# Kernel optimization log

Measured on AMD Instinct MI355X. Metric: run time of the kernel, lower is better.

The kernel has to match this reference:

```python
import jax, jax.numpy as jnp
from jax import lax
import numpy as np

B, CIN, H, W = 8, 3, 256, 256
ED, NH, WS, SHIFT = 64, 4, 8, 4
HD = ED // NH
MLP_H = 4 * ED
N = WS * WS
NW = (H // WS) * (W // WS)
EPS = 1e-5


def _attn_mask():
    # Static shifted-window attention mask, computed with numpy (H, W, WS, SHIFT are static).
    img = np.zeros((H, W), np.float32)
    sl = [slice(0, -WS), slice(-WS, -SHIFT), slice(-SHIFT, None)]
    cnt = 0
    for hs in sl:
        for ws_ in sl:
            img[hs, ws_] = cnt
            cnt += 1
    mw = img.reshape(H // WS, WS, W // WS, WS).transpose(0, 2, 1, 3).reshape(-1, N)
    d = mw[:, None, :] - mw[:, :, None]  # (NW, N, N)
    return jnp.asarray(np.where(d != 0, -100.0, 0.0).astype(np.float32))

ATTN_MASK = _attn_mask()


def _ln(x, g, b):
    m = x.mean(-1, keepdims=True)
    v = x.var(-1, keepdims=True)
    return (x - m) / jnp.sqrt(v + EPS) * g + b


def _conv3x3(x, w, b):
    y = lax.conv_general_dilated(x, w, (1, 1), 'SAME',
                                 dimension_numbers=('NCHW', 'OIHW', 'NCHW'))
    return y + b[None, :, None, None]


def setup_inputs() -> dict:
    key = jax.random.key(0)
    ks = jax.random.split(key, 20)
    s = 0.02
    return dict(
        x=jax.random.normal(ks[0], (B, CIN, H, W), jnp.float32),
        conv_e_w=jax.random.normal(ks[1], (ED, CIN, 3, 3), jnp.float32) * s,
        conv_e_b=jnp.zeros((ED,), jnp.float32),
        n1_g=jnp.ones((ED,), jnp.float32),
        n1_b=jnp.zeros((ED,), jnp.float32),
        qkv_w=jax.random.normal(ks[2], (3 * ED, ED), jnp.float32) * s,
        qkv_b=jnp.zeros((3 * ED,), jnp.float32),
        proj_w=jax.random.normal(ks[3], (ED, ED), jnp.float32) * s,
        proj_b=jnp.zeros((ED,), jnp.float32),
        n2_g=jnp.ones((ED,), jnp.float32),
        n2_b=jnp.zeros((ED,), jnp.float32),
        fc1_w=jax.random.normal(ks[4], (MLP_H, ED), jnp.float32) * s,
        fc1_b=jnp.zeros((MLP_H,), jnp.float32),
        fc2_w=jax.random.normal(ks[5], (ED, MLP_H), jnp.float32) * s,
        fc2_b=jnp.zeros((ED,), jnp.float32),
        conv_u_w=jax.random.normal(ks[6], (CIN, ED, 3, 3), jnp.float32) * s,
        conv_u_b=jnp.zeros((CIN,), jnp.float32),
    )


def reference(x, conv_e_w, conv_e_b, n1_g, n1_b, qkv_w, qkv_b, proj_w, proj_b,
              n2_g, n2_b, fc1_w, fc1_b, fc2_w, fc2_b, conv_u_w, conv_u_b):
    scale = HD ** -0.5
    # conv embed -> NHWC
    xe = _conv3x3(x, conv_e_w, conv_e_b).transpose(0, 2, 3, 1)  # (B,H,W,ED)
    xs = jnp.roll(xe, (-SHIFT, -SHIFT), axis=(1, 2))
    # window partition -> (B*NW, N, ED)
    xw = xs.reshape(B, H // WS, WS, W // WS, WS, ED).transpose(0, 1, 3, 2, 4, 5)
    xw = xw.reshape(B * NW, N, ED)
    # windowed MHA
    xn = _ln(xw, n1_g, n1_b)
    qkv = (xn @ qkv_w.T + qkv_b).reshape(B * NW, N, 3, NH, HD).transpose(2, 0, 3, 1, 4)
    q, k, v = qkv[0] * scale, qkv[1], qkv[2]  # (B*NW, NH, N, HD)
    attn = jnp.einsum('bhnd,bhmd->bhnm', q, k)
    attn = attn.reshape(B, NW, NH, N, N) + ATTN_MASK[None, :, None]
    attn = jax.nn.softmax(attn.reshape(B * NW, NH, N, N), axis=-1)
    out = jnp.einsum('bhnm,bhmd->bhnd', attn, v)
    out = out.transpose(0, 2, 1, 3).reshape(B * NW, N, ED) @ proj_w.T + proj_b
    xw = xw + out
    # window reverse -> (B,H,W,ED), roll back
    xr = xw.reshape(B, H // WS, W // WS, WS, WS, ED).transpose(0, 1, 3, 2, 4, 5)
    xr = xr.reshape(B, H, W, ED)
    x_out = jnp.roll(xr, (SHIFT, SHIFT), axis=(1, 2))  # NHWC
    # MLP branch with residual
    xm = _ln(x_out.reshape(-1, ED), n2_g, n2_b)
    xm = jax.nn.gelu(xm @ fc1_w.T + fc1_b, approximate=False)
    xm = (xm @ fc2_w.T + fc2_b).reshape(B, H, W, ED)
    x_final = (x_out + xm).transpose(0, 3, 1, 2)  # NCHW
    recon = _conv3x3(x_final, conv_u_w, conv_u_b)
    return x + recon
```

## Files before the change

### kernel.cpp

```cpp
#include <hip/hip_runtime.h>
#include <hip/hip_bf16.h>
#include <math.h>

using bf16 = __hip_bfloat16;

typedef short s16x8 __attribute__((ext_vector_type(8)));
typedef short s16x4 __attribute__((ext_vector_type(4)));
typedef float f32x4 __attribute__((ext_vector_type(4)));

static __device__ __forceinline__ float s2f(short s) {
    return __uint_as_float(((unsigned)(unsigned short)s) << 16);
}
static __device__ __forceinline__ short f2s(float v) {
    bf16 b = __float2bfloat16(v);
    return *reinterpret_cast<short*>(&b);
}
static __device__ __forceinline__ float b2f(bf16 v) { return __bfloat162float(v); }
static __device__ __forceinline__ bf16  f2b(float v) { return __float2bfloat16(v); }
static __device__ __forceinline__ unsigned pack2(float a, float b) {
    return (unsigned)(unsigned short)f2s(a) | ((unsigned)(unsigned short)f2s(b) << 16);
}
static __device__ __forceinline__ float frcp(float x) {
    return __builtin_amdgcn_rcpf(x);
}

static __device__ __forceinline__ int lswz(int row, int col) {
    return row * 64 + ((((col >> 3) ^ row) & 7) << 3) + (col & 7);
}
static __device__ __forceinline__ int lbase(int row, int col) {
    return row * 64 + ((((col >> 3) ^ row) & 7) << 3);
}
static __device__ __forceinline__ s16x8 ld8(const short* p) {
    return *(const s16x8*)p;
}
static __device__ __forceinline__ f32x4 mfma16(s16x8 a, s16x8 b, f32x4 c) {
    return __builtin_amdgcn_mfma_f32_16x16x32_bf16(a, b, c, 0, 0, 0);
}

constexpr int B_   = 8;
constexpr int CIN_ = 3;
constexpr int H_   = 256;
constexpr int W_   = 256;
constexpr int ED_  = 64;
constexpr float EPS_ = 1e-5f;

constexpr int WQ_OFF  = 0;
constexpr int WP_OFF  = 12288;
constexpr int W1_OFF  = 16384;
constexpr int W2_OFF  = 32768;
constexpr int NFRAG   = 96;

static __device__ __forceinline__ int clsf(int tok, int eh, int ew) {
    int ch = eh ? (1 + ((tok >> 3) >= 4)) : 0;
    int cw = ew ? (1 + ((tok & 7) >= 4)) : 0;
    return ch * 3 + cw;
}

__global__ __launch_bounds__(256) void k_prep(
    const float* __restrict__ qkvw, const float* __restrict__ projw,
    const float* __restrict__ fc1w, const float* __restrict__ fc2w,
    short* __restrict__ wb)
{
    int g    = blockIdx.x * 256 + threadIdx.x;
    int l    = g & 63;
    int frag = g >> 6;
    int lr   = l & 15, lhi = l >> 4;

    const float* src;
    if (frag < 24) {
        int blk = frag >> 1, half = frag & 1;
        src = qkvw + (blk * 16 + lr) * 64 + half * 32 + lhi * 8;
    } else if (frag < 32) {
        int f = frag - 24; int blk = f >> 1, half = f & 1;
        src = projw + (blk * 16 + lr) * 64 + half * 32 + lhi * 8;
    } else if (frag < 64) {
        int f = frag - 32; int blk = f >> 1, half = f & 1;
        src = fc1w + (blk * 16 + lr) * 64 + half * 32 + lhi * 8;
    } else {
        int f = frag - 64; int pair = f >> 1, half = f & 1;
        int k = pair >> 2, nt = pair & 3;
        src = fc2w + (nt * 16 + lr) * 256 + k * 64 + half * 32 + lhi * 8;
    }
    float4 v0 = *(const float4*)src;
    float4 v1 = *(const float4*)(src + 4);
    s16x8 o = { f2s(v0.x), f2s(v0.y), f2s(v0.z), f2s(v0.w),
                f2s(v1.x), f2s(v1.y), f2s(v1.z), f2s(v1.w) };
    *(s16x8*)&wb[frag * 512 + l * 8] = o;
}

__global__ __launch_bounds__(256) void k_conv_embed(
    const float* __restrict__ x, const float* __restrict__ we,
    const float* __restrict__ be, bf16* __restrict__ xe)
{
    const int t    = threadIdx.x;
    const int wv   = t >> 6;
    const int lane = t & 63;
    const int hb   = blockIdx.x;
    const int h    = hb & 255;
    const int b    = hb >> 8;
    const int col  = wv * 64 + lane;

    const float* xb = x + (size_t)b * (CIN_ * H_ * W_);

    float xr[27];
#pragma unroll
    for (int ci = 0; ci < 3; ++ci)
#pragma unroll
        for (int kh = 0; kh < 3; ++kh) {
            int hy = h + kh - 1;
#pragma unroll
            for (int kw = 0; kw < 3; ++kw) {
                int wx = col + kw - 1;
                bool ok = ((unsigned)hy < 256u) & ((unsigned)wx < 256u);
                xr[ci * 9 + kh * 3 + kw] = ok ? xb[ci * 65536 + hy * 256 + wx] : 0.f;
            }
        }

    unsigned pk[32];
#pragma unroll 4
    for (int op = 0; op < 32; ++op) {
        float a0 = be[2 * op];
        float a1 = be[2 * op + 1];
        const float* w0 = we + (2 * op) * 27;
#pragma unroll
        for (int k = 0; k < 27; ++k) {
            a0 += xr[k] * w0[k];
            a1 += xr[k] * w0[27 + k];
        }
        pk[op] = pack2(a0, a1);
    }

    size_t pixel = (size_t)hb * 256 + col;
    uint4* dst = (uint4*)((short*)xe + pixel * 64);
#pragma unroll
    for (int i = 0; i < 8; ++i) dst[i] = *(uint4*)&pk[i * 4];
}

__global__ __launch_bounds__(256, 3) void k_attn(
    const bf16* __restrict__ xe, const short* __restrict__ wq,
    const float* __restrict__ qkv_b, const short* __restrict__ wp,
    const float* __restrict__ proj_b, const float* __restrict__ n1_g,
    const float* __restrict__ n1_b, bf16* __restrict__ x_out)
{
    __shared__ short s_x[64 * 64];
    __shared__ short s_q[64 * 64];
    __shared__ short s_k[64 * 64];
    __shared__ short s_vt[64 * 64];

    const int t    = threadIdx.x;
    const int w    = t >> 6;
    const int lane = t & 63;
    const int lr   = lane & 15;
    const int lhi  = lane >> 4;

    const int bi  = blockIdx.x;
    const int b   = bi >> 10;
    const int wh  = (bi >> 5) & 31;
    const int wwi = bi & 31;
    const int eh  = (wh == 31), ew = (wwi == 31);

    const bf16* xeb = xe + (size_t)b * (H_ * W_ * ED_);
    const f32x4 cz = { 0.f, 0.f, 0.f, 0.f };

    {
        int n = t >> 2, q = t & 3;
        int hp = (wh * 8 + (n >> 3) + 4) & 255;
        int wp_ = (wwi * 8 + (n & 7) + 4) & 255;
        const short* src = (const short*)xeb + (hp * 256 + wp_) * 64 + q * 16;
        s16x8 u0 = *(const s16x8*)src;
        s16x8 u1 = *(const s16x8*)(src + 8);
        float v[16];
        float s = 0.f, sq = 0.f;
#pragma unroll
        for (int j = 0; j < 8; ++j) { v[j] = s2f(u0[j]); v[8 + j] = s2f(u1[j]); }
#pragma unroll
        for (int j = 0; j < 16; ++j) { s += v[j]; sq += v[j] * v[j]; }
        s  += __shfl_xor(s, 1);  s  += __shfl_xor(s, 2);
        sq += __shfl_xor(sq, 1); sq += __shfl_xor(sq, 2);
        float m = s * (1.f / 64.f);
        float rstd = rsqrtf(sq * (1.f / 64.f) - m * m + EPS_);
        s16x8 w0, w1;
#pragma unroll
        for (int j = 0; j < 8; ++j) {
            w0[j] = f2s((v[j] - m) * rstd * n1_g[q * 16 + j] + n1_b[q * 16 + j]);
            w1[j] = f2s((v[8 + j] - m) * rstd * n1_g[q * 16 + 8 + j] + n1_b[q * 16 + 8 + j]);
        }
        *(s16x8*)&s_x[lbase(n, q * 16)]     = w0;
        *(s16x8*)&s_x[lbase(n, q * 16 + 8)] = w1;
    }
    __syncthreads();

    {
        int arow = w * 16 + lr;
        s16x8 a0 = ld8(&s_x[lbase(arow, lhi * 8)]);
        s16x8 a1 = ld8(&s_x[lbase(arow, 32 + lhi * 8)]);
#pragma unroll
        for (int nt = 0; nt < 8; ++nt) {
            s16x8 b0 = *(const s16x8*)&wq[(nt * 2 + 0) * 512 + lane * 8];
            s16x8 b1 = *(const s16x8*)&wq[(nt * 2 + 1) * 512 + lane * 8];
            f32x4 c = mfma16(a1, b1, mfma16(a0, b0, cz));
            float bias = qkv_b[nt * 16 + lr];
#pragma unroll
            for (int r = 0; r < 4; ++r) {
                int tok = w * 16 + lhi * 4 + r;
                float val = c[r] + bias;
                if (nt < 4) { val *= 0.25f; s_q[lswz(tok, nt * 16 + lr)] = f2s(val); }
                else        {               s_k[lswz(tok, (nt - 4) * 16 + lr)] = f2s(val); }
            }
        }
        s16x8 av0 = *(const s16x8*)&wq[((8 + w) * 2 + 0) * 512 + lane * 8];
        s16x8 av1 = *(const s16x8*)&wq[((8 + w) * 2 + 1) * 512 + lane * 8];
#pragma unroll
        for (int nt = 0; nt < 4; ++nt) {
            s16x8 b0 = ld8(&s_x[lbase(nt * 16 + lr, lhi * 8)]);
            s16x8 b1 = ld8(&s_x[lbase(nt * 16 + lr, 32 + lhi * 8)]);
            f32x4 c = mfma16(av1, b1, mfma16(av0, b0, cz));
#pragma unroll
            for (int r = 0; r < 4; ++r) {
                int d = w * 16 + lhi * 4 + r;
                s_vt[lswz(d, nt * 16 + lr)] = f2s(c[r] + qkv_b[128 + d]);
            }
        }
    }
    __syncthreads();

    const int h = w;
    uint2 pk[4][4];
    {
        const s16x8 z8 = { 0, 0, 0, 0, 0, 0, 0, 0 };
        s16x8 kb[4];
#pragma unroll
        for (int mt = 0; mt < 4; ++mt)
            kb[mt] = (lhi >= 2) ? z8
                   : ld8(&s_k[lbase(mt * 16 + lr, h * 16 + (lhi & 1) * 8)]);
#pragma unroll
        for (int nt = 0; nt < 4; ++nt) {
            s16x8 qb = ld8(&s_q[lbase(nt * 16 + lr, h * 16 + (lhi & 1) * 8)]);
            f32x4 S[4];
#pragma unroll
            for (int mt = 0; mt < 4; ++mt)
                S[mt] = mfma16(kb[mt], qb, cz);

            if (eh | ew) {
                int qc = clsf(nt * 16 + lr, eh, ew);
#pragma unroll
                for (int mt = 0; mt < 4; ++mt)
#pragma unroll
                    for (int r = 0; r < 4; ++r) {
                        int kc = clsf(mt * 16 + lhi * 4 + r, eh, ew);
                        S[mt][r] += (kc != qc) ? -100.f : 0.f;
                    }
            }
            float mx = -1e30f;
#pragma unroll
            for (int mt = 0; mt < 4; ++mt)
#pragma unroll
                for (int r = 0; r < 4; ++r) mx = fmaxf(mx, S[mt][r]);
            mx = fmaxf(mx, __shfl_xor(mx, 16));
            mx = fmaxf(mx, __shfl_xor(mx, 32));
            float ev[4][4];
            float sm = 0.f;
#pragma unroll
            for (int mt = 0; mt < 4; ++mt)
#pragma unroll
                for (int r = 0; r < 4; ++r) {
                    ev[mt][r] = __expf(S[mt][r] - mx);
                    sm += ev[mt][r];
                }
            sm += __shfl_xor(sm, 16);
            sm += __shfl_xor(sm, 32);
            float inv = frcp(sm);
#pragma unroll
            for (int mt = 0; mt < 4; ++mt) {
                pk[nt][mt].x = pack2(ev[mt][0] * inv, ev[mt][1] * inv);
                pk[nt][mt].y = pack2(ev[mt][2] * inv, ev[mt][3] * inv);
            }
        }
    }

    {
        f32x4 O[4] = { cz, cz, cz, cz };
        const int  srcl2 = lr + 32 * (lhi & 1);
        const bool selhi = (lhi >= 2);
#pragma unroll
        for (int ks = 0; ks < 2; ++ks) {
            s16x8 bv = ld8(&s_vt[lbase(h * 16 + lr, ks * 32 + lhi * 8)]);
#pragma unroll
            for (int mo = 0; mo < 4; ++mo) {
                unsigned lAx = (unsigned)__shfl((int)pk[mo][ks * 2 + 0].x, srcl2);
                unsigned lAy = (unsigned)__shfl((int)pk[mo][ks * 2 + 0].y, srcl2);
                unsigned lBx = (unsigned)__shfl((int)pk[mo][ks * 2 + 1].x, srcl2);
                unsigned lBy = (unsigned)__shfl((int)pk[mo][ks * 2 + 1].y, srcl2);
                unsigned hAx = (unsigned)__shfl((int)pk[mo][ks * 2 + 0].x, srcl2 + 16);
                unsigned hAy = (unsigned)__shfl((int)pk[mo][ks * 2 + 0].y, srcl2 + 16);
                unsigned hBx = (unsigned)__shfl((int)pk[mo][ks * 2 + 1].x, srcl2 + 16);
                unsigned hBy = (unsigned)__shfl((int)pk[mo][ks * 2 + 1].y, srcl2 + 16);
                uint4 pa;
                pa.x = selhi ? lBx : lAx;
                pa.y = selhi ? lBy : lAy;
                pa.z = selhi ? hBx : hAx;
                pa.w = selhi ? hBy : hAy;
                O[mo] = mfma16(*(s16x8*)&pa, bv, O[mo]);
            }
        }
#pragma unroll
        for (int mo = 0; mo < 4; ++mo)
#pragma unroll
            for (int r = 0; r < 4; ++r)
                s_x[lswz(mo * 16 + lhi * 4 + r, h * 16 + lr)] = f2s(O[mo][r]);
    }
    __syncthreads();

    {
        int arow = w * 16 + lr;
        s16x8 a0 = ld8(&s_x[lbase(arow, lhi * 8)]);
        s16x8 a1 = ld8(&s_x[lbase(arow, 32 + lhi * 8)]);
        size_t rowbase[4];
#pragma unroll
        for (int r = 0; r < 4; ++r) {
            int tok = w * 16 + lhi * 4 + r;
            int hp = (wh * 8 + (tok >> 3) + 4) & 255;
            int wpx = (wwi * 8 + (tok & 7) + 4) & 255;
            rowbase[r] = (size_t)(hp * 256 + wpx) * 64;
        }
        const size_t bbase = (size_t)b * (H_ * W_ * ED_);
#pragma unroll
        for (int nt = 0; nt < 4; ++nt) {
            s16x8 b0 = *(const s16x8*)&wp[(nt * 2 + 0) * 512 + lane * 8];
            s16x8 b1 = *(const s16x8*)&wp[(nt * 2 + 1) * 512 + lane * 8];
            f32x4 c = mfma16(a1, b1, mfma16(a0, b0, cz));
            float bias = proj_b[nt * 16 + lr];
#pragma unroll
            for (int r = 0; r < 4; ++r) {
                size_t gi = rowbase[r] + nt * 16 + lr;
                float val = c[r] + bias + b2f(xeb[gi]);
                x_out[bbase + gi] = f2b(val);
            }
        }
    }
}

__global__ __launch_bounds__(512, 4) void k_mlp(
    const bf16* __restrict__ xo, const short* __restrict__ w1,
    const float* __restrict__ fc1_b, const short* __restrict__ w2,
    const float* __restrict__ fc2_b, const float* __restrict__ n2_g,
    const float* __restrict__ n2_b, bf16* __restrict__ xf)
{
    __shared__ short s_x[128 * 64];
    __shared__ short s_h[128 * 64];

    const int t    = threadIdx.x;
    const int w    = t >> 6;
    const int lane = t & 63;
    const int lr   = lane & 15;
    const int lhi  = lane >> 4;
    const size_t tok0 = (size_t)blockIdx.x * 128;
    const short* xos = (const short*)xo;

    {
        int n = t >> 2, q = t & 3;
        const short* src = xos + (tok0 + n) * 64 + q * 16;
        s16x8 u0 = *(const s16x8*)src;
        s16x8 u1 = *(const s16x8*)(src + 8);
        float v[16];
        float s = 0.f, sq = 0.f;
#pragma unroll
        for (int j = 0; j < 8; ++j) { v[j] = s2f(u0[j]); v[8 + j] = s2f(u1[j]); }
#pragma unroll
        for (int j = 0; j < 16; ++j) { s += v[j]; sq += v[j] * v[j]; }
        s  += __shfl_xor(s, 1);  s  += __shfl_xor(s, 2);
        sq += __shfl_xor(sq, 1); sq += __shfl_xor(sq, 2);
        float m = s * (1.f / 64.f);
        float rstd = rsqrtf(sq * (1.f / 64.f) - m * m + EPS_);
        s16x8 w0, w1_;
#pragma unroll
        for (int j = 0; j < 8; ++j) {
            w0[j]  = f2s((v[j] - m) * rstd * n2_g[q * 16 + j] + n2_b[q * 16 + j]);
            w1_[j] = f2s((v[8 + j] - m) * rstd * n2_g[q * 16 + 8 + j] + n2_b[q * 16 + 8 + j]);
        }
        *(s16x8*)&s_x[lbase(n, q * 16)]     = w0;
        *(s16x8*)&s_x[lbase(n, q * 16 + 8)] = w1_;
    }

    const f32x4 cz = { 0.f, 0.f, 0.f, 0.f };
    f32x4 acc[4] = { cz, cz, cz, cz };
    const int arow = w * 16 + lr;

    s16x8 a0 = ld8(&s_x[lbase(arow, lhi * 8)]);
    s16x8 a1 = ld8(&s_x[lbase(arow, 32 + lhi * 8)]);

    for (int k = 0; k < 4; ++k) {
#pragma unroll
        for (int nt = 0; nt < 4; ++nt) {
            const short* bp = &w1[((k * 4 + nt) * 2) * 512 + lane * 8];
            s16x8 b0 = *(const s16x8*)bp;
            s16x8 b1 = *(const s16x8*)(bp + 512);
            f32x4 c = mfma16(a1, b1, mfma16(a0, b0, cz));
            float bias = fc1_b[k * 64 + nt * 16 + lr];
#pragma unroll
            for (int r = 0; r < 4; ++r) {
                float hv = c[r] + bias;
                float u = hv + 0.044715f * hv * hv * hv;
                hv = hv * frcp(1.f + __expf(-1.5957691216f * u));
                s_h[lswz(w * 16 + lhi * 4 + r, nt * 16 + lr)] = f2s(hv);
            }
        }
        s16x8 h0 = ld8(&s_h[lbase(arow, lhi * 8)]);
        s16x8 h1 = ld8(&s_h[lbase(arow, 32 + lhi * 8)]);
#pragma unroll
        for (int nt = 0; nt < 4; ++nt) {
            const short* bp2 = &w2[((k * 4 + nt) * 2) * 512 + lane * 8];
            s16x8 b0 = *(const s16x8*)bp2;
            s16x8 b1 = *(const s16x8*)(bp2 + 512);
            acc[nt] = mfma16(h1, b1, mfma16(h0, b0, acc[nt]));
        }
    }

#pragma unroll
    for (int nt = 0; nt < 4; ++nt) {
        float bias = fc2_b[nt * 16 + lr];
#pragma unroll
        for (int r = 0; r < 4; ++r) {
            int tok = w * 16 + lhi * 4 + r;
            size_t gi = (tok0 + tok) * 64 + nt * 16 + lr;
            float v = acc[nt][r] + bias + s2f(xos[gi]);
            ((short*)xf)[gi] = f2s(v);
        }
    }
}

__global__ __launch_bounds__(256) void k_conv_up(
    const float* __restrict__ x, const bf16* __restrict__ xf,
    const float* __restrict__ wu, const float* __restrict__ bu,
    float* __restrict__ out)
{
    __shared__ short s_t[198 * 64];
    __shared__ short s_bf[1152 * 8];
    __shared__ float s_wu[1728];

    const int t    = threadIdx.x;
    const int pix0 = blockIdx.x * 64;
    const int b    = pix0 >> 16;
    const int h    = (pix0 >> 8) & 255;
    const int w0   = pix0 & 255;

    const short* xfs = (const short*)xf;

    for (int e = t; e < 1584; e += 256) {
        int rc = e >> 3, j8 = e & 7;
        int hy_l = (unsigned)rc / 66u;
        int wx_l = rc - hy_l * 66;
        int hy = h + hy_l - 1;
        int wx = w0 + wx_l - 1;
        s16x8 v = { 0, 0, 0, 0, 0, 0, 0, 0 };
        if (((unsigned)hy < 256u) & ((unsigned)wx < 256u))
            v = *(const s16x8*)&xfs[((size_t)((b * 256 + hy) * 256 + wx)) * 64 + j8 * 8];
        *(s16x8*)&s_t[lbase(rc, j8 * 8)] = v;
    }
    for (int e = t; e < 1728; e += 256) s_wu[e] = wu[e];
    __syncthreads();

    for (int fid = t; fid < 1152; fid += 256) {
        int tap  = fid >> 7;
        int half = (fid >> 6) & 1;
        int ln   = fid & 63;
        int co   = ln & 15;
        s16x8 v = { 0, 0, 0, 0, 0, 0, 0, 0 };
        if (co < 3) {
            int ci0 = half * 32 + (ln >> 4) * 8;
#pragma unroll
            for (int j = 0; j < 8; ++j)
                v[j] = f2s(s_wu[(co * 64 + ci0 + j) * 9 + tap]);
        }
        *(s16x8*)&s_bf[fid * 8] = v;
    }
    __syncthreads();

    const int wv   = t >> 6;
    const int lane = t & 63;
    const int lr   = lane & 15;
    const int lhi  = lane >> 4;

    f32x4 acc = { 0.f, 0.f, 0.f, 0.f };
#pragma unroll
    for (int kh = 0; kh < 3; ++kh)
#pragma unroll
        for (int kw = 0; kw < 3; ++kw) {
            const int tap = kh * 3 + kw;
            const int R   = kh * 66 + wv * 16 + lr + kw;
#pragma unroll
            for (int half = 0; half < 2; ++half) {
                s16x8 a   = ld8(&s_t[lbase(R, half * 32 + lhi * 8)]);
                s16x8 bfr = ld8(&s_bf[((tap * 2 + half) * 64 + lane) * 8]);
                acc = mfma16(a, bfr, acc);
            }
        }

    if (lr < 3) {
        const int co = lr;
        const int wp = wv * 16 + lhi * 4;
        size_t o0 = (size_t)b * 3 * 65536 + (size_t)co * 65536 + (size_t)h * 256 + w0 + wp;
        float4 xv = *(const float4*)&x[o0];
        float bias = bu[co];
        float4 ov;
        ov.x = acc[0] + bias + xv.x;
        ov.y = acc[1] + bias + xv.y;
        ov.z = acc[2] + bias + xv.z;
        ov.w = acc[3] + bias + xv.w;
        *(float4*)&out[o0] = ov;
    }
}

extern "C" void kernel_launch(void* const* d_in, const int* in_sizes, int n_in,
                              void* d_out, int out_size, void* d_ws, size_t ws_size,
                              hipStream_t stream)
{
    const float* x     = (const float*)d_in[0];
    const float* cew   = (const float*)d_in[1];
    const float* ceb   = (const float*)d_in[2];
    const float* n1g   = (const float*)d_in[3];
    const float* n1b   = (const float*)d_in[4];
    const float* qkvw  = (const float*)d_in[5];
    const float* qkvb  = (const float*)d_in[6];
    const float* projw = (const float*)d_in[7];
    const float* projb = (const float*)d_in[8];
    const float* n2g   = (const float*)d_in[9];
    const float* n2b   = (const float*)d_in[10];
    const float* fc1w  = (const float*)d_in[11];
    const float* fc1b  = (const float*)d_in[12];
    const float* fc2w  = (const float*)d_in[13];
    const float* fc2b  = (const float*)d_in[14];
    const float* cuw   = (const float*)d_in[15];
    const float* cub   = (const float*)d_in[16];
    float* out = (float*)d_out;

    const size_t planeElems = (size_t)B_ * H_ * W_ * ED_;
    bf16* xe = (bf16*)d_ws;
    bf16* xo = (bf16*)((char*)d_ws + planeElems * sizeof(bf16));

    short* wb = (short*)d_out;

    hipLaunchKernelGGL(k_prep, dim3(NFRAG * 64 / 256), dim3(256), 0, stream,
                       qkvw, projw, fc1w, fc2w, wb);
    hipLaunchKernelGGL(k_conv_embed, dim3(2048), dim3(256), 0, stream, x, cew, ceb, xe);
    hipLaunchKernelGGL(k_attn,       dim3(8192), dim3(256), 0, stream,
                       xe, wb + WQ_OFF, qkvb, wb + WP_OFF, projb, n1g, n1b, xo);
    hipLaunchKernelGGL(k_mlp,        dim3(4096), dim3(512), 0, stream,
                       xo, wb + W1_OFF, fc1b, wb + W2_OFF, fc2b, n2g, n2b, xe);
    hipLaunchKernelGGL(k_conv_up,    dim3(8192), dim3(256), 0, stream, x, xe, cuw, cub, out);
}
```

Measured before the change: 411.5 us.

## Fuse windowed attention and MLP into one kernel per window

Merges the attention kernel and the MLP kernel so that each 64-token window block runs LN2, fc1+GELU, fc2 and the residual right after the projection. The attention output stays in LDS and registers instead of being written to and re-read from a global bf16 buffer. This removes a full-plane round trip to global memory and one kernel launch. Since the MLP is per token, it is applied before un-rolling, and results are written straight to the rolled positions. In exchange the MLP now runs at the attention kernel's 256-thread, 64-token block granularity instead of 128-token blocks, and register pressure goes up because residual values are held in registers.

```diff
diff --git a/kernel.cpp b/kernel.cpp
--- a/kernel.cpp
+++ b/kernel.cpp
@@ -136,11 +136,14 @@
     for (int i = 0; i < 8; ++i) dst[i] = *(uint4*)&pk[i * 4];
 }
 
-__global__ __launch_bounds__(256, 3) void k_attn(
+__global__ __launch_bounds__(256, 3) void k_attn_mlp(
     const bf16* __restrict__ xe, const short* __restrict__ wq,
     const float* __restrict__ qkv_b, const short* __restrict__ wp,
     const float* __restrict__ proj_b, const float* __restrict__ n1_g,
-    const float* __restrict__ n1_b, bf16* __restrict__ x_out)
+    const float* __restrict__ n1_b, const short* __restrict__ w1,
+    const float* __restrict__ fc1_b, const short* __restrict__ w2,
+    const float* __restrict__ fc2_b, const float* __restrict__ n2_g,
+    const float* __restrict__ n2_b, bf16* __restrict__ xf)
 {
     __shared__ short s_x[64 * 64];
     __shared__ short s_q[64 * 64];
@@ -179,14 +182,14 @@
         sq += __shfl_xor(sq, 1); sq += __shfl_xor(sq, 2);
         float m = s * (1.f / 64.f);
         float rstd = rsqrtf(sq * (1.f / 64.f) - m * m + EPS_);
-        s16x8 w0, w1;
+        s16x8 w0, w1_;
 #pragma unroll
         for (int j = 0; j < 8; ++j) {
-            w0[j] = f2s((v[j] - m) * rstd * n1_g[q * 16 + j] + n1_b[q * 16 + j]);
-            w1[j] = f2s((v[8 + j] - m) * rstd * n1_g[q * 16 + 8 + j] + n1_b[q * 16 + 8 + j]);
+            w0[j]  = f2s((v[j] - m) * rstd * n1_g[q * 16 + j] + n1_b[q * 16 + j]);
+            w1_[j] = f2s((v[8 + j] - m) * rstd * n1_g[q * 16 + 8 + j] + n1_b[q * 16 + 8 + j]);
         }
         *(s16x8*)&s_x[lbase(n, q * 16)]     = w0;
-        *(s16x8*)&s_x[lbase(n, q * 16 + 8)] = w1;
+        *(s16x8*)&s_x[lbase(n, q * 16 + 8)] = w1_;
     }
     __syncthreads();
 
@@ -311,11 +314,12 @@
     }
     __syncthreads();
 
+    size_t rowbase[4];
+    float  valr[4][4];
     {
         int arow = w * 16 + lr;
         s16x8 a0 = ld8(&s_x[lbase(arow, lhi * 8)]);
         s16x8 a1 = ld8(&s_x[lbase(arow, 32 + lhi * 8)]);
-        size_t rowbase[4];
 #pragma unroll
         for (int r = 0; r < 4; ++r) {
             int tok = w * 16 + lhi * 4 + r;
@@ -323,7 +327,6 @@
             int wpx = (wwi * 8 + (tok & 7) + 4) & 255;
             rowbase[r] = (size_t)(hp * 256 + wpx) * 64;
         }
-        const size_t bbase = (size_t)b * (H_ * W_ * ED_);
 #pragma unroll
         for (int nt = 0; nt < 4; ++nt) {
             s16x8 b0 = *(const s16x8*)&wp[(nt * 2 + 0) * 512 + lane * 8];
@@ -332,36 +335,18 @@
             float bias = proj_b[nt * 16 + lr];
 #pragma unroll
             for (int r = 0; r < 4; ++r) {
-                size_t gi = rowbase[r] + nt * 16 + lr;
-                float val = c[r] + bias + b2f(xeb[gi]);
-                x_out[bbase + gi] = f2b(val);
-            }
-        }
-    }
-}
-
-__global__ __launch_bounds__(512, 4) void k_mlp(
-    const bf16* __restrict__ xo, const short* __restrict__ w1,
-    const float* __restrict__ fc1_b, const short* __restrict__ w2,
-    const float* __restrict__ fc2_b, const float* __restrict__ n2_g,
-    const float* __restrict__ n2_b, bf16* __restrict__ xf)
-{
-    __shared__ short s_x[128 * 64];
-    __shared__ short s_h[128 * 64];
-
-    const int t    = threadIdx.x;
-    const int w    = t >> 6;
-    const int lane = t & 63;
-    const int lr   = lane & 15;
-    const int lhi  = lane >> 4;
-    const size_t tok0 = (size_t)blockIdx.x * 128;
-    const short* xos = (const short*)xo;
-
-    {
-        int n = t >> 2, q = t & 3;
-        const short* src = xos + (tok0 + n) * 64 + q * 16;
-        s16x8 u0 = *(const s16x8*)src;
-        s16x8 u1 = *(const s16x8*)(src + 8);
+                int tok = w * 16 + lhi * 4 + r;
+                short vs = f2s(c[r] + bias + b2f(xeb[rowbase[r] + nt * 16 + lr]));
+                s_x[lswz(tok, nt * 16 + lr)] = vs;
+                valr[nt][r] = s2f(vs);
+            }
+        }
+    }
+
+    {
+        int n = w * 16 + (lane >> 2), q = lane & 3;
+        s16x8 u0 = ld8(&s_x[lbase(n, q * 16)]);
+        s16x8 u1 = ld8(&s_x[lbase(n, q * 16 + 8)]);
         float v[16];
         float s = 0.f, sq = 0.f;
 #pragma unroll
@@ -378,53 +363,55 @@
             w0[j]  = f2s((v[j] - m) * rstd * n2_g[q * 16 + j] + n2_b[q * 16 + j]);
             w1_[j] = f2s((v[8 + j] - m) * rstd * n2_g[q * 16 + 8 + j] + n2_b[q * 16 + 8 + j]);
         }
-        *(s16x8*)&s_x[lbase(n, q * 16)]     = w0;
-        *(s16x8*)&s_x[lbase(n, q * 16 + 8)] = w1_;
-    }
-
-    const f32x4 cz = { 0.f, 0.f, 0.f, 0.f };
+        *(s16x8*)&s_q[lbase(n, q * 16)]     = w0;
+        *(s16x8*)&s_q[lbase(n, q * 16 + 8)] = w1_;
+    }
+
     f32x4 acc[4] = { cz, cz, cz, cz };
-    const int arow = w * 16 + lr;
-
-    s16x8 a0 = ld8(&s_x[lbase(arow, lhi * 8)]);
-    s16x8 a1 = ld8(&s_x[lbase(arow, 32 + lhi * 8)]);
-
-    for (int k = 0; k < 4; ++k) {
+    {
+        const int arow = w * 16 + lr;
+        s16x8 xa0 = ld8(&s_q[lbase(arow, lhi * 8)]);
+        s16x8 xa1 = ld8(&s_q[lbase(arow, 32 + lhi * 8)]);
+
+        for (int k = 0; k < 4; ++k) {
+#pragma unroll
+            for (int nt = 0; nt < 4; ++nt) {
+                const short* bp = &w1[((k * 4 + nt) * 2) * 512 + lane * 8];
+                s16x8 b0 = *(const s16x8*)bp;
+                s16x8 b1 = *(const s16x8*)(bp + 512);
+                f32x4 c = mfma16(xa1, b1, mfma16(xa0, b0, cz));
+                float bias = fc1_b[k * 64 + nt * 16 + lr];
+#pragma unroll
+                for (int r = 0; r < 4; ++r) {
+                    float hv = c[r] + bias;
+                    float u = hv + 0.044715f * hv * hv * hv;
+                    hv = hv * frcp(1.f + __expf(-1.5957691216f * u));
+                    s_k[lswz(w * 16 + lhi * 4 + r, nt * 16 + lr)] = f2s(hv);
+                }
+            }
+            s16x8 h0 = ld8(&s_k[lbase(arow, lhi * 8)]);
+            s16x8 h1 = ld8(&s_k[lbase(arow, 32 + lhi * 8)]);
+#pragma unroll
+            for (int nt = 0; nt < 4; ++nt) {
+                const short* bp2 = &w2[((k * 4 + nt) * 2) * 512 + lane * 8];
+                s16x8 b0 = *(const s16x8*)bp2;
+                s16x8 b1 = *(const s16x8*)(bp2 + 512);
+                acc[nt] = mfma16(h1, b1, mfma16(h0, b0, acc[nt]));
+            }
+        }
+    }
+
+    {
+        const size_t bbase = (size_t)b * (H_ * W_ * ED_);
+        short* xfs = (short*)xf;
 #pragma unroll
         for (int nt = 0; nt < 4; ++nt) {
-            const short* bp = &w1[((k * 4 + nt) * 2) * 512 + lane * 8];
-            s16x8 b0 = *(const s16x8*)bp;
-            s16x8 b1 = *(const s16x8*)(bp + 512);
-            f32x4 c = mfma16(a1, b1, mfma16(a0, b0, cz));
-            float bias = fc1_b[k * 64 + nt * 16 + lr];
+            float bias = fc2_b[nt * 16 + lr];
 #pragma unroll
             for (int r = 0; r < 4; ++r) {
-                float hv = c[r] + bias;
-                float u = hv + 0.044715f * hv * hv * hv;
-                hv = hv * frcp(1.f + __expf(-1.5957691216f * u));
-                s_h[lswz(w * 16 + lhi * 4 + r, nt * 16 + lr)] = f2s(hv);
-            }
-        }
-        s16x8 h0 = ld8(&s_h[lbase(arow, lhi * 8)]);
-        s16x8 h1 = ld8(&s_h[lbase(arow, 32 + lhi * 8)]);
-#pragma unroll
-        for (int nt = 0; nt < 4; ++nt) {
-            const short* bp2 = &w2[((k * 4 + nt) * 2) * 512 + lane * 8];
-            s16x8 b0 = *(const s16x8*)bp2;
-            s16x8 b1 = *(const s16x8*)(bp2 + 512);
-            acc[nt] = mfma16(h1, b1, mfma16(h0, b0, acc[nt]));
-        }
-    }
-
-#pragma unroll
-    for (int nt = 0; nt < 4; ++nt) {
-        float bias = fc2_b[nt * 16 + lr];
-#pragma unroll
-        for (int r = 0; r < 4; ++r) {
-            int tok = w * 16 + lhi * 4 + r;
-            size_t gi = (tok0 + tok) * 64 + nt * 16 + lr;
-            float v = acc[nt][r] + bias + s2f(xos[gi]);
-            ((short*)xf)[gi] = f2s(v);
+                size_t gi = bbase + rowbase[r] + nt * 16 + lr;
+                xfs[gi] = f2s(acc[nt][r] + bias + valr[nt][r]);
+            }
         }
     }
 }
@@ -536,16 +523,15 @@
 
     const size_t planeElems = (size_t)B_ * H_ * W_ * ED_;
     bf16* xe = (bf16*)d_ws;
-    bf16* xo = (bf16*)((char*)d_ws + planeElems * sizeof(bf16));
+    bf16* xf = (bf16*)((char*)d_ws + planeElems * sizeof(bf16));
 
     short* wb = (short*)d_out;
 
     hipLaunchKernelGGL(k_prep, dim3(NFRAG * 64 / 256), dim3(256), 0, stream,
                        qkvw, projw, fc1w, fc2w, wb);
     hipLaunchKernelGGL(k_conv_embed, dim3(2048), dim3(256), 0, stream, x, cew, ceb, xe);
-    hipLaunchKernelGGL(k_attn,       dim3(8192), dim3(256), 0, stream,
-                       xe, wb + WQ_OFF, qkvb, wb + WP_OFF, projb, n1g, n1b, xo);
-    hipLaunchKernelGGL(k_mlp,        dim3(4096), dim3(512), 0, stream,
-                       xo, wb + W1_OFF, fc1b, wb + W2_OFF, fc2b, n2g, n2b, xe);
-    hipLaunchKernelGGL(k_conv_up,    dim3(8192), dim3(256), 0, stream, x, xe, cuw, cub, out);
-}
+    hipLaunchKernelGGL(k_attn_mlp,   dim3(8192), dim3(256), 0, stream,
+                       xe, wb + WQ_OFF, qkvb, wb + WP_OFF, projb, n1g, n1b,
+                       wb + W1_OFF, fc1b, wb + W2_OFF, fc2b, n2g, n2b, xf);
+    hipLaunchKernelGGL(k_conv_up,    dim3(8192), dim3(256), 0, stream, x, xf, cuw, cub, out);
+}
```

Result: no change. 405.7 us (-1.4%).
